# Optimization experiments

Measured on AMD Instinct MI355X. Metric: run time of the kernel, lower is better.

The kernel has to match this reference:

```python
import jax, jax.numpy as jnp
import numpy as np

D_EMB = 768
N_HEADS = 12
D_K = D_EMB // N_HEADS


def setup_inputs() -> dict:
    key = jax.random.key(0)
    k0, k1, k2, k3, k4 = jax.random.split(key, 5)
    B, S = 2, 4096
    scale = 1.0 / np.sqrt(D_EMB)
    return {
        "inputs": jax.random.normal(k0, (B, S, D_EMB), dtype=jnp.float32),
        "Wq": jax.random.normal(k1, (D_EMB, D_EMB), dtype=jnp.float32) * scale,
        "Wk": jax.random.normal(k2, (D_EMB, D_EMB), dtype=jnp.float32) * scale,
        "Wv": jax.random.normal(k3, (D_EMB, D_EMB), dtype=jnp.float32) * scale,
        "Wo": jax.random.normal(k4, (D_EMB, D_EMB), dtype=jnp.float32) * scale,
    }


def reference(inputs, Wq, Wk, Wv, Wo):
    B, S, _ = inputs.shape
    def split_heads(x):  # [B,S,E] -> [B,H,S,dk]
        return x.reshape(B, S, N_HEADS, D_K).transpose(0, 2, 1, 3)
    q = split_heads(inputs @ Wq)
    k = split_heads(inputs @ Wk)
    v = split_heads(inputs @ Wv)
    scores = jnp.einsum("bhqd,bhkd->bhqk", q, k) / jnp.sqrt(
        jnp.asarray(D_K, dtype=inputs.dtype)
    )
    attn = jax.nn.softmax(scores, axis=-1)
    out = jnp.einsum("bhqk,bhkd->bhqd", attn, v)
    out = out.transpose(0, 2, 1, 3).reshape(B, S, D_EMB)
    return out @ Wo
```

## Files before the change

kernel.cpp:

```cpp
#include <hip/hip_runtime.h>

#define D_EMB 768
#define NH 12
#define DK 64
#define NB 2
#define SS 4096
#define E3 (3*D_EMB)
#define MM (NB*SS)

typedef unsigned short u16;
typedef __attribute__((ext_vector_type(8))) __bf16 bf16x8;
typedef __attribute__((ext_vector_type(4))) float f32x4;
typedef __attribute__((ext_vector_type(4))) unsigned int u32x4;

static __device__ __forceinline__ u16 f2bf(float f) {
  unsigned u = __builtin_bit_cast(unsigned, f);
  u += 0x7fffu + ((u >> 16) & 1u);
  return (u16)(u >> 16);
}
static __device__ __forceinline__ f32x4 mfma16(bf16x8 a, bf16x8 b, f32x4 c) {
  return __builtin_amdgcn_mfma_f32_16x16x32_bf16(a, b, c, 0, 0, 0);
}
static __device__ __forceinline__ float exp2_fast(float x) {
#if __has_builtin(__builtin_amdgcn_exp2f)
  return __builtin_amdgcn_exp2f(x);
#else
  return __builtin_exp2f(x);
#endif
}
static __device__ __forceinline__ float rcp_fast(float x) {
#if __has_builtin(__builtin_amdgcn_rcpf)
  return __builtin_amdgcn_rcpf(x);
#else
  return 1.f / x;
#endif
}
static __device__ __forceinline__ void gload_lds16(const u16* g, u16* l) {
  __builtin_amdgcn_global_load_lds((const __attribute__((address_space(1))) void*)g,
                                   (__attribute__((address_space(3))) void*)l, 16, 0, 0);
}

__global__ __launch_bounds__(256) void cast_kernel(const float* __restrict__ in,
                                                   u16* __restrict__ out, int n) {
  int i = (blockIdx.x * 256 + threadIdx.x) * 4;
  if (i + 3 < n) {
    float4 v = *(const float4*)(in + i);
    out[i + 0] = f2bf(v.x);
    out[i + 1] = f2bf(v.y);
    out[i + 2] = f2bf(v.z);
    out[i + 3] = f2bf(v.w);
  }
}

__global__ __launch_bounds__(256) void transpose_cast_all(const float* __restrict__ Wq,
                                                          const float* __restrict__ Wk,
                                                          const float* __restrict__ Wv,
                                                          const float* __restrict__ Wo,
                                                          u16* __restrict__ WTqkv,
                                                          u16* __restrict__ WoT, float qscale) {
  __shared__ float tile[32][33];
  int z = blockIdx.z;
  const float* W = (z == 0) ? Wq : (z == 1) ? Wk : (z == 2) ? Wv : Wo;
  u16* WT = (z < 3) ? WTqkv + (size_t)z * D_EMB * D_EMB : WoT;
  float scale = (z == 0) ? qscale : 1.0f;
  int kb = blockIdx.y * 32, nb = blockIdx.x * 32;
  int tx = threadIdx.x, ty = threadIdx.y;
#pragma unroll
  for (int i = 0; i < 4; i++)
    tile[ty + i * 8][tx] = W[(size_t)(kb + ty + i * 8) * D_EMB + nb + tx];
  __syncthreads();
#pragma unroll
  for (int i = 0; i < 4; i++)
    WT[(size_t)(nb + ty + i * 8) * D_EMB + kb + tx] = f2bf(tile[tx][ty + i * 8] * scale);
}

__global__ __launch_bounds__(256) void transpose_v(const u16* __restrict__ QKV,
                                                   u16* __restrict__ VT) {
  __shared__ u16 tile[32][33];
  int bh = blockIdx.z;
  int b = bh / NH, h = bh % NH;
  int sb = blockIdx.x * 32, db = blockIdx.y * 32;
  int tx = threadIdx.x, ty = threadIdx.y;
  const u16* src = QKV + (size_t)(b * SS) * E3 + 2 * D_EMB + h * DK;
  u16* dst = VT + (size_t)bh * DK * SS;
#pragma unroll
  for (int i = 0; i < 4; i++)
    tile[ty + i * 8][tx] = src[(size_t)(sb + ty + i * 8) * E3 + db + tx];
  __syncthreads();
  int s = sb + tx;
  int k6 = s & 63;
  int p = (s & ~63) | (k6 & 0x23) | ((k6 & 0x0C) << 1) | ((k6 & 0x10) >> 2);
#pragma unroll
  for (int i = 0; i < 4; i++)
    dst[(size_t)(db + ty + i * 8) * SS + p] = tile[tx][ty + i * 8];
}

template <int OUTF32>
__global__ __launch_bounds__(256) void gemm_bt(const u16* __restrict__ A,
                                               const u16* __restrict__ Bt,
                                               void* __restrict__ Cout,
                                               int M, int N, int K, float scale) {
  __shared__ __align__(16) u16 As[128 * 32];
  __shared__ __align__(16) u16 Bs[128 * 32];
  int tid = threadIdx.x;
  int wave = tid >> 6, lane = tid & 63;
  int g = lane >> 4, nIdx = lane & 15;
  int m0 = blockIdx.y * 128, n0 = blockIdx.x * 128;
  int wm = (wave >> 1) * 64, wn = (wave & 1) * 64;

  f32x4 acc[4][4] = {};

  int row = tid >> 2, co = (tid & 3) * 8;
  int row2 = row + 64;

  for (int k0 = 0; k0 < K; k0 += 32) {
    __syncthreads();
    gload_lds16(A  + (size_t)(m0 + row)  * K + k0 + co, As + row  * 32 + co);
    gload_lds16(Bt + (size_t)(n0 + row)  * K + k0 + co, Bs + row  * 32 + co);
    gload_lds16(A  + (size_t)(m0 + row2) * K + k0 + co, As + row2 * 32 + co);
    gload_lds16(Bt + (size_t)(n0 + row2) * K + k0 + co, Bs + row2 * 32 + co);
    __syncthreads();

    bf16x8 af[4], bfr[4];
#pragma unroll
    for (int i = 0; i < 4; i++)
      af[i] = *(const bf16x8*)(As + (wm + i * 16 + nIdx) * 32 + g * 8);
#pragma unroll
    for (int j = 0; j < 4; j++)
      bfr[j] = *(const bf16x8*)(Bs + (wn + j * 16 + nIdx) * 32 + g * 8);
#pragma unroll
    for (int i = 0; i < 4; i++)
#pragma unroll
      for (int j = 0; j < 4; j++)
        acc[i][j] = mfma16(af[i], bfr[j], acc[i][j]);
  }

#pragma unroll
  for (int i = 0; i < 4; i++)
#pragma unroll
    for (int j = 0; j < 4; j++)
#pragma unroll
      for (int r = 0; r < 4; r++) {
        int rr = m0 + wm + i * 16 + g * 4 + r;
        int cc = n0 + wn + j * 16 + nIdx;
        float v = acc[i][j][r] * scale;
        if (OUTF32)
          ((float*)Cout)[(size_t)rr * N + cc] = v;
        else
          ((u16*)Cout)[(size_t)rr * N + cc] = f2bf(v);
      }
}

__global__ __launch_bounds__(256, 3) void flash(const u16* __restrict__ QKV,
                                                const u16* __restrict__ VT,
                                                u16* __restrict__ O) {
  __shared__ __align__(16) u16 smem[17408];

  int b = blockIdx.z, h = blockIdx.y;
  int q0 = blockIdx.x * 128;
  int tid = threadIdx.x, w = tid >> 6, l = tid & 63;
  int g = l >> 4, n = l & 15;
  int qh = w & 1, st = w >> 1;

  const u16* VTb = VT + (size_t)(b * NH + h) * DK * SS;
  u16* sbase = smem + st * 8192;

  const u16* Qbase = QKV + (size_t)(b * SS + q0 + qh * 64) * E3 + h * DK;
  bf16x8 qf[4][2];
#pragma unroll
  for (int qg = 0; qg < 4; qg++)
#pragma unroll
    for (int hf = 0; hf < 2; hf++)
      qf[qg][hf] = *(const bf16x8*)(Qbase + (size_t)(qg * 16 + n) * E3 + hf * 32 + g * 8);

  f32x4 o_acc[4][4] = {};
  float lsum[4] = {0.f, 0.f, 0.f, 0.f};
  u32x4 onev = {0x3F803F80u, 0x3F803F80u, 0x3F803F80u, 0x3F803F80u};
  bf16x8 aone = __builtin_bit_cast(bf16x8, onev);

  int rL = l >> 3, cL = l & 7;
  const u16* g0;
  size_t rstep, tstep;
  u16* sd0;
  if ((w & 1) == 0) {
    g0 = QKV + ((size_t)(b * SS) + st * 2048 + rL) * E3 + D_EMB + h * DK + (cL ^ rL) * 8;
    rstep = (size_t)8 * E3;
    tstep = (size_t)32 * E3;
    sd0 = sbase + l * 8;
  } else {
    g0 = VTb + (size_t)(l >> 2) * SS + st * 2048 + ((l & 3) ^ ((l >> 3) & 3)) * 8;
    rstep = (size_t)16 * SS;
    tstep = 32;
    sd0 = sbase + 2048 + l * 8;
  }

#pragma unroll
  for (int i = 0; i < 4; i++)
    gload_lds16(g0 + i * rstep, sd0 + i * 512);

  int xrn = n & 7;
  int xv = (n >> 1) & 3;
  for (int kt = 0; kt < 64; kt++) {
    __syncthreads();

    const u16* pK = sbase + (kt & 1) * 4096;
    const u16* pV = pK + 2048;

    if (kt < 63) {
      const u16* gn = g0 + (size_t)(kt + 1) * tstep;
      u16* sd = sd0 + ((kt + 1) & 1) * 4096;
#pragma unroll
      for (int i = 0; i < 4; i++)
        gload_lds16(gn + i * rstep, sd + i * 512);
    }

    bf16x8 kf[2][2];
#pragma unroll
    for (int jj = 0; jj < 2; jj++)
#pragma unroll
      for (int hf = 0; hf < 2; hf++)
        kf[jj][hf] = *(const bf16x8*)(pK + (jj * 16 + n) * 64 + ((hf * 4 + g) ^ xrn) * 8);

#pragma unroll
    for (int p = 0; p < 2; p++) {
      f32x4 C[2][2];
#pragma unroll
      for (int q2 = 0; q2 < 2; q2++) {
        int qg = 2 * p + q2;
#pragma unroll
        for (int jj = 0; jj < 2; jj++) {
          f32x4 t = {};
          t = mfma16(kf[jj][0], qf[qg][0], t);
          t = mfma16(kf[jj][1], qf[qg][1], t);
          C[q2][jj] = t;
        }
      }
      u32x4 Bw[2];
#pragma unroll
      for (int q2 = 0; q2 < 2; q2++)
#pragma unroll
        for (int jj = 0; jj < 2; jj++) {
          float p0 = exp2_fast(C[q2][jj][0]);
          float p1 = exp2_fast(C[q2][jj][1]);
          float p2 = exp2_fast(C[q2][jj][2]);
          float p3 = exp2_fast(C[q2][jj][3]);
          Bw[q2][jj * 2] = __builtin_amdgcn_perm(__builtin_bit_cast(unsigned, p1),
                                                 __builtin_bit_cast(unsigned, p0), 0x07060302u);
          Bw[q2][jj * 2 + 1] = __builtin_amdgcn_perm(__builtin_bit_cast(unsigned, p3),
                                                     __builtin_bit_cast(unsigned, p2), 0x07060302u);
        }
#pragma unroll
      for (int q2 = 0; q2 < 2; q2++) {
        f32x4 z = {};
        z = mfma16(aone, __builtin_bit_cast(bf16x8, Bw[q2]), z);
        lsum[2 * p + q2] += z[0];
      }
#pragma unroll
      for (int dt = 0; dt < 4; dt++) {
        bf16x8 vf = *(const bf16x8*)(pV + (dt * 16 + n) * 32 + (g ^ xv) * 8);
#pragma unroll
        for (int q2 = 0; q2 < 2; q2++)
          o_acc[2 * p + q2][dt] = mfma16(vf, __builtin_bit_cast(bf16x8, Bw[q2]),
                                         o_acc[2 * p + q2][dt]);
      }
    }
  }

  __syncthreads();

  float* dumpF = (float*)smem;
  if (w >= 2) {
    float* dst = dumpF + ((size_t)((w - 2) * 64 + l)) * 68;
#pragma unroll
    for (int qg = 0; qg < 4; qg++)
#pragma unroll
      for (int dt = 0; dt < 4; dt++)
        *(f32x4*)(dst + (qg * 4 + dt) * 4) = o_acc[qg][dt];
    f32x4 lv = {lsum[0], lsum[1], lsum[2], lsum[3]};
    *(f32x4*)(dst + 64) = lv;
  }
  __syncthreads();
  if (w < 2) {
    float* src = dumpF + ((size_t)(w * 64 + l)) * 68;
#pragma unroll
    for (int qg = 0; qg < 4; qg++)
#pragma unroll
      for (int dt = 0; dt < 4; dt++)
        o_acc[qg][dt] += *(f32x4*)(src + (qg * 4 + dt) * 4);
    f32x4 lv = *(f32x4*)(src + 64);
#pragma unroll
    for (int qg = 0; qg < 4; qg++) {
      float rl = rcp_fast(lsum[qg] + lv[qg]);
      u16* Obp = O + (size_t)(b * SS + q0 + w * 64 + qg * 16 + n) * D_EMB + h * DK;
#pragma unroll
      for (int dt = 0; dt < 4; dt++) {
        uint2 pk;
        pk.x = (unsigned)f2bf(o_acc[qg][dt][0] * rl) |
               ((unsigned)f2bf(o_acc[qg][dt][1] * rl) << 16);
        pk.y = (unsigned)f2bf(o_acc[qg][dt][2] * rl) |
               ((unsigned)f2bf(o_acc[qg][dt][3] * rl) << 16);
        *(uint2*)(Obp + dt * 16 + g * 4) = pk;
      }
    }
  }
}

extern "C" void kernel_launch(void* const* d_in, const int* in_sizes, int n_in,
                              void* d_out, int out_size, void* d_ws, size_t ws_size,
                              hipStream_t stream) {
  const float* X  = (const float*)d_in[0];
  const float* Wq = (const float*)d_in[1];
  const float* Wk = (const float*)d_in[2];
  const float* Wv = (const float*)d_in[3];
  const float* Wo = (const float*)d_in[4];
  float* out = (float*)d_out;

  u16* Xb    = (u16*)d_ws;
  u16* WTqkv = Xb + (size_t)MM * D_EMB;
  u16* WoT   = WTqkv + (size_t)E3 * D_EMB;
  u16* QKV   = WoT + (size_t)D_EMB * D_EMB;
  u16* VT    = QKV + (size_t)MM * E3;
  u16* Ob    = VT + (size_t)NB * NH * DK * SS;

  dim3 tb(32, 8);
  cast_kernel<<<(MM * D_EMB) / 1024, 256, 0, stream>>>(X, Xb, MM * D_EMB);
  transpose_cast_all<<<dim3(24, 24, 4), tb, 0, stream>>>(Wq, Wk, Wv, Wo, WTqkv, WoT,
                                                         0.125f * 1.4426950408889634f);
  gemm_bt<0><<<dim3(E3 / 128, MM / 128), 256, 0, stream>>>(Xb, WTqkv, (void*)QKV,
                                                           MM, E3, D_EMB, 1.0f);
  transpose_v<<<dim3(SS / 32, 2, NB * NH), tb, 0, stream>>>(QKV, VT);
  flash<<<dim3(SS / 128, NH, NB), 256, 0, stream>>>(QKV, VT, Ob);
  gemm_bt<1><<<dim3(D_EMB / 128, MM / 128), 256, 0, stream>>>(Ob, WoT, (void*)out,
                                                              MM, D_EMB, D_EMB, 1.0f);
}
```

Before: 266.3 us.

## Fuse V transpose into QKV GEMM epilogue and unroll flash loop by two

The QKV projection GEMM now writes the V columns directly into the transposed, permuted VT layout, so the separate transpose_v kernel and its launch go away. The V part of QKV is no longer written row-major, and flash only reads V through VT. The flash key loop is manually unrolled by two with fixed double-buffer addresses and precomputed swizzle offsets, which removes per-iteration buffer-index arithmetic and the prefetch branch. The trade-off is that the GEMM epilogue for V now does scattered 2-byte stores along SS and carries extra index math per element.

```diff
diff --git a/kernel.cpp b/kernel.cpp
--- a/kernel.cpp
+++ b/kernel.cpp
@@ -74,31 +74,11 @@
     WT[(size_t)(nb + ty + i * 8) * D_EMB + kb + tx] = f2bf(tile[tx][ty + i * 8] * scale);
 }
 
-__global__ __launch_bounds__(256) void transpose_v(const u16* __restrict__ QKV,
-                                                   u16* __restrict__ VT) {
-  __shared__ u16 tile[32][33];
-  int bh = blockIdx.z;
-  int b = bh / NH, h = bh % NH;
-  int sb = blockIdx.x * 32, db = blockIdx.y * 32;
-  int tx = threadIdx.x, ty = threadIdx.y;
-  const u16* src = QKV + (size_t)(b * SS) * E3 + 2 * D_EMB + h * DK;
-  u16* dst = VT + (size_t)bh * DK * SS;
-#pragma unroll
-  for (int i = 0; i < 4; i++)
-    tile[ty + i * 8][tx] = src[(size_t)(sb + ty + i * 8) * E3 + db + tx];
-  __syncthreads();
-  int s = sb + tx;
-  int k6 = s & 63;
-  int p = (s & ~63) | (k6 & 0x23) | ((k6 & 0x0C) << 1) | ((k6 & 0x10) >> 2);
-#pragma unroll
-  for (int i = 0; i < 4; i++)
-    dst[(size_t)(db + ty + i * 8) * SS + p] = tile[tx][ty + i * 8];
-}
-
 template <int OUTF32>
 __global__ __launch_bounds__(256) void gemm_bt(const u16* __restrict__ A,
                                                const u16* __restrict__ Bt,
                                                void* __restrict__ Cout,
+                                               u16* __restrict__ VTout,
                                                int M, int N, int K, float scale) {
   __shared__ __align__(16) u16 As[128 * 32];
   __shared__ __align__(16) u16 Bs[128 * 32];
@@ -135,6 +115,7 @@
         acc[i][j] = mfma16(af[i], bfr[j], acc[i][j]);
   }
 
+  bool vmode = (VTout != nullptr) && (n0 >= 1536);
 #pragma unroll
   for (int i = 0; i < 4; i++)
 #pragma unroll
@@ -144,11 +125,73 @@
         int rr = m0 + wm + i * 16 + g * 4 + r;
         int cc = n0 + wn + j * 16 + nIdx;
         float v = acc[i][j][r] * scale;
-        if (OUTF32)
+        if (OUTF32) {
           ((float*)Cout)[(size_t)rr * N + cc] = v;
-        else
+        } else if (vmode) {
+          int hd = cc - 1536;
+          int h = hd >> 6, d = hd & 63;
+          int bb = rr >> 12, s = rr & 4095;
+          int k6 = s & 63;
+          int p = (s & ~63) | (k6 & 0x23) | ((k6 & 0x0C) << 1) | ((k6 & 0x10) >> 2);
+          VTout[((size_t)(bb * NH + h) * DK + d) * SS + p] = f2bf(v);
+        } else {
           ((u16*)Cout)[(size_t)rr * N + cc] = f2bf(v);
+        }
       }
+}
+
+static __device__ __forceinline__ void flash_compute(
+    const u16* pK, const u16* pV, int n, int xk0, int xk1, int xvv,
+    bf16x8 (&qf)[4][2], f32x4 (&o_acc)[4][4], float (&lsum)[4], bf16x8 aone) {
+  bf16x8 kf[2][2];
+#pragma unroll
+  for (int jj = 0; jj < 2; jj++) {
+    kf[jj][0] = *(const bf16x8*)(pK + (jj * 16 + n) * 64 + xk0);
+    kf[jj][1] = *(const bf16x8*)(pK + (jj * 16 + n) * 64 + xk1);
+  }
+#pragma unroll
+  for (int p = 0; p < 2; p++) {
+    f32x4 C[2][2];
+#pragma unroll
+    for (int q2 = 0; q2 < 2; q2++) {
+      int qg = 2 * p + q2;
+#pragma unroll
+      for (int jj = 0; jj < 2; jj++) {
+        f32x4 t = {};
+        t = mfma16(kf[jj][0], qf[qg][0], t);
+        t = mfma16(kf[jj][1], qf[qg][1], t);
+        C[q2][jj] = t;
+      }
+    }
+    u32x4 Bw[2];
+#pragma unroll
+    for (int q2 = 0; q2 < 2; q2++)
+#pragma unroll
+      for (int jj = 0; jj < 2; jj++) {
+        float p0 = exp2_fast(C[q2][jj][0]);
+        float p1 = exp2_fast(C[q2][jj][1]);
+        float p2 = exp2_fast(C[q2][jj][2]);
+        float p3 = exp2_fast(C[q2][jj][3]);
+        Bw[q2][jj * 2] = __builtin_amdgcn_perm(__builtin_bit_cast(unsigned, p1),
+                                               __builtin_bit_cast(unsigned, p0), 0x07060302u);
+        Bw[q2][jj * 2 + 1] = __builtin_amdgcn_perm(__builtin_bit_cast(unsigned, p3),
+                                                   __builtin_bit_cast(unsigned, p2), 0x07060302u);
+      }
+#pragma unroll
+    for (int q2 = 0; q2 < 2; q2++) {
+      f32x4 z = {};
+      z = mfma16(aone, __builtin_bit_cast(bf16x8, Bw[q2]), z);
+      lsum[2 * p + q2] += z[0];
+    }
+#pragma unroll
+    for (int dt = 0; dt < 4; dt++) {
+      bf16x8 vf = *(const bf16x8*)(pV + (dt * 16 + n) * 32 + xvv);
+#pragma unroll
+      for (int q2 = 0; q2 < 2; q2++)
+        o_acc[2 * p + q2][dt] = mfma16(vf, __builtin_bit_cast(bf16x8, Bw[q2]),
+                                       o_acc[2 * p + q2][dt]);
+    }
+  }
 }
 
 __global__ __launch_bounds__(256, 3) void flash(const u16* __restrict__ QKV,
@@ -199,71 +242,31 @@
     gload_lds16(g0 + i * rstep, sd0 + i * 512);
 
   int xrn = n & 7;
-  int xv = (n >> 1) & 3;
-  for (int kt = 0; kt < 64; kt++) {
+  int xk0 = (g ^ xrn) * 8;
+  int xk1 = xk0 ^ 32;
+  int xvv = (g ^ ((n >> 1) & 3)) * 8;
+
+  for (int kt = 0; kt < 64; kt += 2) {
     __syncthreads();
-
-    const u16* pK = sbase + (kt & 1) * 4096;
-    const u16* pV = pK + 2048;
-
-    if (kt < 63) {
+    {
       const u16* gn = g0 + (size_t)(kt + 1) * tstep;
-      u16* sd = sd0 + ((kt + 1) & 1) * 4096;
-#pragma unroll
-      for (int i = 0; i < 4; i++)
-        gload_lds16(gn + i * rstep, sd + i * 512);
-    }
-
-    bf16x8 kf[2][2];
-#pragma unroll
-    for (int jj = 0; jj < 2; jj++)
-#pragma unroll
-      for (int hf = 0; hf < 2; hf++)
-        kf[jj][hf] = *(const bf16x8*)(pK + (jj * 16 + n) * 64 + ((hf * 4 + g) ^ xrn) * 8);
-
-#pragma unroll
-    for (int p = 0; p < 2; p++) {
-      f32x4 C[2][2];
-#pragma unroll
-      for (int q2 = 0; q2 < 2; q2++) {
-        int qg = 2 * p + q2;
-#pragma unroll
-        for (int jj = 0; jj < 2; jj++) {
-          f32x4 t = {};
-          t = mfma16(kf[jj][0], qf[qg][0], t);
-          t = mfma16(kf[jj][1], qf[qg][1], t);
-          C[q2][jj] = t;
-        }
-      }
-      u32x4 Bw[2];
-#pragma unroll
-      for (int q2 = 0; q2 < 2; q2++)
-#pragma unroll
-        for (int jj = 0; jj < 2; jj++) {
-          float p0 = exp2_fast(C[q2][jj][0]);
-          float p1 = exp2_fast(C[q2][jj][1]);
-          float p2 = exp2_fast(C[q2][jj][2]);
-          float p3 = exp2_fast(C[q2][jj][3]);
-          Bw[q2][jj * 2] = __builtin_amdgcn_perm(__builtin_bit_cast(unsigned, p1),
-                                                 __builtin_bit_cast(unsigned, p0), 0x07060302u);
-          Bw[q2][jj * 2 + 1] = __builtin_amdgcn_perm(__builtin_bit_cast(unsigned, p3),
-                                                     __builtin_bit_cast(unsigned, p2), 0x07060302u);
-        }
-#pragma unroll
-      for (int q2 = 0; q2 < 2; q2++) {
-        f32x4 z = {};
-        z = mfma16(aone, __builtin_bit_cast(bf16x8, Bw[q2]), z);
-        lsum[2 * p + q2] += z[0];
-      }
-#pragma unroll
-      for (int dt = 0; dt < 4; dt++) {
-        bf16x8 vf = *(const bf16x8*)(pV + (dt * 16 + n) * 32 + (g ^ xv) * 8);
-#pragma unroll
-        for (int q2 = 0; q2 < 2; q2++)
-          o_acc[2 * p + q2][dt] = mfma16(vf, __builtin_bit_cast(bf16x8, Bw[q2]),
-                                         o_acc[2 * p + q2][dt]);
-      }
-    }
+      u16* sd = sd0 + 4096;
+      gload_lds16(gn + 0 * rstep, sd + 0 * 512);
+      gload_lds16(gn + 1 * rstep, sd + 1 * 512);
+      gload_lds16(gn + 2 * rstep, sd + 2 * 512);
+      gload_lds16(gn + 3 * rstep, sd + 3 * 512);
+    }
+    flash_compute(sbase, sbase + 2048, n, xk0, xk1, xvv, qf, o_acc, lsum, aone);
+
+    __syncthreads();
+    if (kt < 62) {
+      const u16* gn = g0 + (size_t)(kt + 2) * tstep;
+      gload_lds16(gn + 0 * rstep, sd0 + 0 * 512);
+      gload_lds16(gn + 1 * rstep, sd0 + 1 * 512);
+      gload_lds16(gn + 2 * rstep, sd0 + 2 * 512);
+      gload_lds16(gn + 3 * rstep, sd0 + 3 * 512);
+    }
+    flash_compute(sbase + 4096, sbase + 4096 + 2048, n, xk0, xk1, xvv, qf, o_acc, lsum, aone);
   }
 
   __syncthreads();
@@ -326,10 +329,9 @@
   cast_kernel<<<(MM * D_EMB) / 1024, 256, 0, stream>>>(X, Xb, MM * D_EMB);
   transpose_cast_all<<<dim3(24, 24, 4), tb, 0, stream>>>(Wq, Wk, Wv, Wo, WTqkv, WoT,
                                                          0.125f * 1.4426950408889634f);
-  gemm_bt<0><<<dim3(E3 / 128, MM / 128), 256, 0, stream>>>(Xb, WTqkv, (void*)QKV,
+  gemm_bt<0><<<dim3(E3 / 128, MM / 128), 256, 0, stream>>>(Xb, WTqkv, (void*)QKV, VT,
                                                            MM, E3, D_EMB, 1.0f);
-  transpose_v<<<dim3(SS / 32, 2, NB * NH), tb, 0, stream>>>(QKV, VT);
   flash<<<dim3(SS / 128, NH, NB), 256, 0, stream>>>(QKV, VT, Ob);
-  gemm_bt<1><<<dim3(D_EMB / 128, MM / 128), 256, 0, stream>>>(Ob, WoT, (void*)out,
+  gemm_bt<1><<<dim3(D_EMB / 128, MM / 128), 256, 0, stream>>>(Ob, WoT, (void*)out, nullptr,
                                                               MM, D_EMB, D_EMB, 1.0f);
 }
```

Result: slower. 303.9 us (+14.1%).
